# Kernel optimization log

Measured on AMD Instinct MI355X. Metric: run time of the kernel, lower is better.

The kernel has to match this reference:

```python
import jax, jax.numpy as jnp
import numpy as np

B, P, K = 128, 1024, 4  # 128 clouds of 1024 points, kNN k=4 (includes self, as PyG knn does)


def _edge_mlp(e, W1, b1, W2, b2):
    # PyG MLP([2d, c, c]) with plain_last=True: ReLU after first linear only;
    # batch-norm at init (running_mean=0, var=1) is identity in eval mode.
    h = jax.nn.relu(e @ W1 + b1)
    return h @ W2 + b2


def _dynamic_edge_conv(x, W1, b1, W2, b2):
    # x: [B, P, d]. Recompute kNN graph in feature space per cloud, build edge
    # features [x_i, x_j - x_i], apply MLP, max-aggregate over neighbors.
    sq = jnp.sum(x * x, axis=-1)  # [B,P]
    dist = sq[:, :, None] + sq[:, None, :] - 2.0 * jnp.einsum('bid,bjd->bij', x, x)  # [B,P,P]
    _, idx = jax.lax.top_k(-dist, K)  # [B,P,K] nearest neighbors (self included, dist 0)
    xj = jax.vmap(lambda xc, ic: xc[ic])(x, idx)  # [B,P,K,d]
    xi = jnp.broadcast_to(x[:, :, None, :], xj.shape)
    e = jnp.concatenate([xi, xj - xi], axis=-1)  # [B,P,K,2d]
    h = _edge_mlp(e, W1, b1, W2, b2)  # [B,P,K,c]
    return jnp.max(h, axis=2)  # max aggregation -> [B,P,c]


def setup_inputs() -> dict:
    key = jax.random.key(0)
    ks = jax.random.split(key, 24)
    s = 0.1
    d = {
        'x': jax.random.normal(ks[0], (B * P, 1), dtype=jnp.float32),
        'batch': (jnp.arange(B * P, dtype=jnp.int32) // P),
        # conv1: MLP([2, 32, 32])
        'c1W1': s * jax.random.normal(ks[1], (2, 32)), 'c1b1': jnp.zeros((32,)),
        'c1W2': s * jax.random.normal(ks[2], (32, 32)), 'c1b2': jnp.zeros((32,)),
        # conv2: MLP([64, 32, 32])
        'c2W1': s * jax.random.normal(ks[3], (64, 32)), 'c2b1': jnp.zeros((32,)),
        'c2W2': s * jax.random.normal(ks[4], (32, 32)), 'c2b2': jnp.zeros((32,)),
        # conv3: MLP([64, 64, 64])
        'c3W1': s * jax.random.normal(ks[5], (64, 64)), 'c3b1': jnp.zeros((64,)),
        'c3W2': s * jax.random.normal(ks[6], (64, 64)), 'c3b2': jnp.zeros((64,)),
        # final MLP([128, 264, 264, 264, 2]), norm=None, dropout inactive in eval
        'mW1': s * jax.random.normal(ks[7], (128, 264)), 'mb1': jnp.zeros((264,)),
        'mW2': s * jax.random.normal(ks[8], (264, 264)), 'mb2': jnp.zeros((264,)),
        'mW3': s * jax.random.normal(ks[9], (264, 264)), 'mb3': jnp.zeros((264,)),
        'mW4': s * jax.random.normal(ks[10], (264, 2)), 'mb4': jnp.zeros((2,)),
    }
    return d


def reference(x, batch, c1W1, c1b1, c1W2, c1b2, c2W1, c2b1, c2W2, c2b2,
              c3W1, c3b1, c3W2, c3b2, mW1, mb1, mW2, mb2, mW3, mb3, mW4, mb4):
    # batch ids are contiguous equal-size groups (arange // P); use reshape.
    xb = x.reshape(B, P, -1)
    x1 = _dynamic_edge_conv(xb, c1W1, c1b1, c1W2, c1b2)  # [B,P,32]
    x2 = _dynamic_edge_conv(x1, c2W1, c2b1, c2W2, c2b2)  # [B,P,32]
    x3 = _dynamic_edge_conv(x2, c3W1, c3b1, c3W2, c3b2)  # [B,P,64]
    f = jnp.concatenate([x1, x2, x3], axis=-1).reshape(B * P, -1)  # [N,128]
    h = jax.nn.relu(f @ mW1 + mb1)
    h = jax.nn.relu(h @ mW2 + mb2)
    h = jax.nn.relu(h @ mW3 + mb3)
    out = h @ mW4 + mb4  # [N,2]
    return jax.nn.log_softmax(out, axis=1)
```

## Files before the change

### kernel.cpp

```cpp
#include <hip/hip_runtime.h>
#include <hip/hip_bf16.h>
#include <float.h>
#include <math.h>

#define BB 128
#define PP 1024
#define KNN 4
#define NROWS (BB * PP)

typedef __bf16 v8bf __attribute__((ext_vector_type(8)));
typedef float  v4f  __attribute__((ext_vector_type(4)));

__device__ inline unsigned short f2bs(float f) {
    __hip_bfloat16 h = __float2bfloat16(f);
    return *(unsigned short*)&h;
}
__device__ inline unsigned packbf2(float a, float b) {
    return (unsigned)f2bs(a) | ((unsigned)f2bs(b) << 16);
}
__device__ inline float bflo(unsigned u) { return __builtin_bit_cast(float, u << 16); }
__device__ inline float bfhi(unsigned u) { return __builtin_bit_cast(float, u & 0xFFFF0000u); }

__global__ __launch_bounds__(256)
void pack_kernel(const float* __restrict__ src, int D,
                 __hip_bfloat16* __restrict__ xh, __hip_bfloat16* __restrict__ xl,
                 float* __restrict__ sq)
{
    const int t = blockIdx.x * 256 + threadIdx.x;
    const int row = t >> 2, part = t & 3;
    float v[8];
    #pragma unroll
    for (int u = 0; u < 8; u++) {
        int d = part * 8 + u;
        v[u] = (d < D) ? src[(size_t)row * D + d] : 0.f;
    }
    float s = 0.f;
    unsigned int hw[4], lw[4];
    #pragma unroll
    for (int w = 0; w < 4; w++) {
        unsigned short h2[2], l2[2];
        #pragma unroll
        for (int e = 0; e < 2; e++) {
            float x = v[2 * w + e];
            __hip_bfloat16 hb = __float2bfloat16(x);
            float hf = __bfloat162float(hb);
            __hip_bfloat16 lb = __float2bfloat16(x - hf);
            h2[e] = *(unsigned short*)&hb;
            l2[e] = *(unsigned short*)&lb;
            s = fmaf(x, x, s);
        }
        hw[w] = (unsigned int)h2[0] | ((unsigned int)h2[1] << 16);
        lw[w] = (unsigned int)l2[0] | ((unsigned int)l2[1] << 16);
    }
    s += __shfl_xor(s, 1);
    s += __shfl_xor(s, 2);
    uint4 hv; hv.x = hw[0]; hv.y = hw[1]; hv.z = hw[2]; hv.w = hw[3];
    uint4 lv; lv.x = lw[0]; lv.y = lw[1]; lv.z = lw[2]; lv.w = lw[3];
    *(uint4*)&xh[(size_t)row * 32 + part * 8] = hv;
    *(uint4*)&xl[(size_t)row * 32 + part * 8] = lv;
    if (part == 0) sq[row] = s;
}

__global__ __launch_bounds__(256, 4)
void knn_mfma(const __hip_bfloat16* __restrict__ xh, const __hip_bfloat16* __restrict__ xl,
              const float* __restrict__ sq, int* __restrict__ nidx)
{
    __shared__ __align__(16) char scb[64 * 512];
    unsigned* cand = (unsigned*)scb;

    const int tid = threadIdx.x;
    const int wv = tid >> 6, lane = tid & 63;
    const int lr = lane & 15, lq = lane >> 4;
    const int b = blockIdx.y, i0 = blockIdx.x * 64;
    const size_t Rb = (size_t)b * PP;

    v8bf ah[4], al[4];
    #pragma unroll
    for (int it = 0; it < 4; it++) {
        size_t g = Rb + i0 + it * 16 + lr;
        ah[it] = __builtin_bit_cast(v8bf, *(const uint4*)(xh + g * 32 + lq * 8));
        al[it] = __builtin_bit_cast(v8bf, *(const uint4*)(xl + g * 32 + lq * 8));
    }

    float sqq[4][4];
    #pragma unroll
    for (int it = 0; it < 4; it++)
        #pragma unroll
        for (int m = 0; m < 4; m++)
            sqq[it][m] = sq[Rb + i0 + it * 16 + lq * 4 + m];

    const int r = tid & 63, qt = tid >> 6;
    unsigned m0 = ~0u, m1 = ~0u, m2 = ~0u, m3 = ~0u;

    for (int ch = 0; ch < 8; ch++) {
        #pragma unroll
        for (int jt2 = 0; jt2 < 2; jt2++) {
            const int tl = wv * 2 + jt2;
            const size_t gj = Rb + ch * 128 + tl * 16 + lr;
            v8bf bh = __builtin_bit_cast(v8bf, *(const uint4*)(xh + gj * 32 + lq * 8));
            v8bf bl = __builtin_bit_cast(v8bf, *(const uint4*)(xl + gj * 32 + lq * 8));
            const float sqv = sq[gj];
            const unsigned jloc = (unsigned)(ch * 128 + tl * 16 + lr);
            const int cb = (tl * 16 + lr) * 4;
            #pragma unroll
            for (int it = 0; it < 4; it++) {
                v4f a = (v4f){0.f, 0.f, 0.f, 0.f};
                a = __builtin_amdgcn_mfma_f32_16x16x32_bf16(al[it], bl, a, 0, 0, 0);
                a = __builtin_amdgcn_mfma_f32_16x16x32_bf16(al[it], bh, a, 0, 0, 0);
                a = __builtin_amdgcn_mfma_f32_16x16x32_bf16(ah[it], bl, a, 0, 0, 0);
                a = __builtin_amdgcn_mfma_f32_16x16x32_bf16(ah[it], bh, a, 0, 0, 0);
                #pragma unroll
                for (int m = 0; m < 4; m++) {
                    float s = fmaf(-2.f, a[m], sqv + sqq[it][m]);
                    s = fmaxf(s, 0.f);
                    unsigned key = (__builtin_bit_cast(unsigned, s) & 0xFFFFFC00u) | jloc;
                    const int row = it * 16 + lq * 4 + m;
                    *(unsigned*)(scb + row * 512 + (cb ^ ((row & 7) << 4))) = key;
                }
            }
        }
        __asm__ volatile("" ::: "memory");
        {
            const int rsw = (r & 7) << 4;
            #pragma unroll
            for (int s8 = 0; s8 < 8; s8++) {
                uint4 kv = *(const uint4*)(scb + r * 512 + ((qt * 128 + s8 * 16) ^ rsw));
                unsigned kk[4] = {kv.x, kv.y, kv.z, kv.w};
                #pragma unroll
                for (int e = 0; e < 4; e++) {
                    unsigned key = kk[e], t;
                    t = min(m0, key); key = max(m0, key); m0 = t;
                    t = min(m1, key); key = max(m1, key); m1 = t;
                    t = min(m2, key); key = max(m2, key); m2 = t;
                    m3 = min(m3, key);
                }
            }
        }
        __asm__ volatile("" ::: "memory");
    }

    __syncthreads();
    cand[(qt * 4 + 0) * 64 + r] = m0;
    cand[(qt * 4 + 1) * 64 + r] = m1;
    cand[(qt * 4 + 2) * 64 + r] = m2;
    cand[(qt * 4 + 3) * 64 + r] = m3;
    __syncthreads();

    if (tid < 64) {
        unsigned g0 = ~0u, g1 = ~0u, g2 = ~0u, g3 = ~0u;
        #pragma unroll
        for (int s2 = 0; s2 < 16; s2++) {
            unsigned key = cand[s2 * 64 + tid], t;
            t = min(g0, key); key = max(g0, key); g0 = t;
            t = min(g1, key); key = max(g1, key); g1 = t;
            t = min(g2, key); key = max(g2, key); g2 = t;
            g3 = min(g3, key);
        }
        const int base = (int)Rb;
        int* op = nidx + (size_t)(Rb + i0 + tid) * KNN;
        op[0] = base + (int)(g0 & 1023u);
        op[1] = base + (int)(g1 & 1023u);
        op[2] = base + (int)(g2 & 1023u);
        op[3] = base + (int)(g3 & 1023u);
    }
}

template<int D, int H, int C, typename OT>
__global__ __launch_bounds__(256, 4)
void edge_mfma(const float* __restrict__ x, const int* __restrict__ nidx,
               const __hip_bfloat16* __restrict__ EW1, const __hip_bfloat16* __restrict__ EW2,
               const float* __restrict__ b1g, const float* __restrict__ b2g,
               OT* __restrict__ out)
{
    constexpr int NE = 256;
    constexpr int TDP = (D == 1) ? 32 : 64;
    constexpr int DP  = TDP / 2;
    constexpr int P   = ((TDP > H) ? TDP : H) + 8;
    constexpr int NT1 = H / 16, NT2 = C / 16;
    constexpr int KS1 = TDP / 32, KS2 = H / 32;

    __shared__ __hip_bfloat16 xe[NE * P];

    const int tid = threadIdx.x;
    const int wv = tid >> 6, lane = tid & 63;
    const int lr = lane & 15, q = lane >> 4;
    const int p0 = blockIdx.x * 64;

    {
        const int e = wv * 64 + lane;
        const int j = nidx[(size_t)p0 * KNN + e];
        const int pi = p0 + (e >> 2);
        if constexpr (D == 1) {
            #pragma unroll
            for (int s = 0; s < P / 8; s++) {
                uint4 z; z.x = 0u; z.y = 0u; z.z = 0u; z.w = 0u;
                *(uint4*)&xe[e * P + s * 8] = z;
            }
            xe[e * P + 0]  = __float2bfloat16(x[pi]);
            xe[e * P + DP] = __float2bfloat16(x[j]);
        } else {
            const float* si = x + (size_t)pi * D;
            const float* sj = x + (size_t)j * D;
            #pragma unroll
            for (int s = 0; s < D / 8; s++) {
                float4 f0 = *(const float4*)&si[s * 8];
                float4 f1 = *(const float4*)&si[s * 8 + 4];
                uint4 uv;
                uv.x = packbf2(f0.x, f0.y); uv.y = packbf2(f0.z, f0.w);
                uv.z = packbf2(f1.x, f1.y); uv.w = packbf2(f1.z, f1.w);
                *(uint4*)&xe[e * P + s * 8] = uv;
            }
            #pragma unroll
            for (int s = 0; s < D / 8; s++) {
                float4 f0 = *(const float4*)&sj[s * 8];
                float4 f1 = *(const float4*)&sj[s * 8 + 4];
                uint4 uv;
                uv.x = packbf2(f0.x, f0.y); uv.y = packbf2(f0.z, f0.w);
                uv.z = packbf2(f1.x, f1.y); uv.w = packbf2(f1.z, f1.w);
                *(uint4*)&xe[e * P + DP + s * 8] = uv;
            }
        }
    }

    v4f acc1[4][NT1];
    #pragma unroll
    for (int mi = 0; mi < 4; mi++)
        #pragma unroll
        for (int nt = 0; nt < NT1; nt++) acc1[mi][nt] = (v4f){0.f, 0.f, 0.f, 0.f};

    #pragma unroll
    for (int ks = 0; ks < KS1; ks++) {
        v8bf a[4];
        #pragma unroll
        for (int mi = 0; mi < 4; mi++)
            a[mi] = __builtin_bit_cast(v8bf,
                *(const uint4*)&xe[(wv * 64 + mi * 16 + lr) * P + ks * 32 + q * 8]);
        v8bf b[NT1];
        #pragma unroll
        for (int nt = 0; nt < NT1; nt++)
            b[nt] = __builtin_bit_cast(v8bf,
                *(const uint4*)(EW1 + (size_t)(nt * 16 + lr) * TDP + ks * 32 + q * 8));
        #pragma unroll
        for (int mi = 0; mi < 4; mi++)
            #pragma unroll
            for (int nt = 0; nt < NT1; nt++)
                acc1[mi][nt] = __builtin_amdgcn_mfma_f32_16x16x32_bf16(a[mi], b[nt], acc1[mi][nt], 0, 0, 0);
    }
    #pragma unroll
    for (int nt = 0; nt < NT1; nt++) {
        const float bias = b1g[nt * 16 + lr];
        #pragma unroll
        for (int mi = 0; mi < 4; mi++) {
            #pragma unroll
            for (int m = 0; m < 4; m++) {
                int row = wv * 64 + mi * 16 + q * 4 + m;
                xe[row * P + nt * 16 + lr] =
                    __float2bfloat16(fmaxf(acc1[mi][nt][m] + bias, 0.f));
            }
        }
    }

    v4f acc2[4][NT2];
    #pragma unroll
    for (int mi = 0; mi < 4; mi++)
        #pragma unroll
        for (int nt = 0; nt < NT2; nt++) acc2[mi][nt] = (v4f){0.f, 0.f, 0.f, 0.f};

    #pragma unroll
    for (int ks = 0; ks < KS2; ks++) {
        v8bf a[4];
        #pragma unroll
        for (int mi = 0; mi < 4; mi++)
            a[mi] = __builtin_bit_cast(v8bf,
                *(const uint4*)&xe[(wv * 64 + mi * 16 + lr) * P + ks * 32 + q * 8]);
        v8bf b[NT2];
        #pragma unroll
        for (int nt = 0; nt < NT2; nt++)
            b[nt] = __builtin_bit_cast(v8bf,
                *(const uint4*)(EW2 + (size_t)(nt * 16 + lr) * H + ks * 32 + q * 8));
        #pragma unroll
        for (int mi = 0; mi < 4; mi++)
            #pragma unroll
            for (int nt = 0; nt < NT2; nt++)
                acc2[mi][nt] = __builtin_amdgcn_mfma_f32_16x16x32_bf16(a[mi], b[nt], acc2[mi][nt], 0, 0, 0);
    }
    #pragma unroll
    for (int nt = 0; nt < NT2; nt++) {
        const int c = nt * 16 + lr;
        const float bias = b2g[c];
        #pragma unroll
        for (int mi = 0; mi < 4; mi++) {
            float v = fmaxf(fmaxf(acc2[mi][nt][0], acc2[mi][nt][1]),
                            fmaxf(acc2[mi][nt][2], acc2[mi][nt][3])) + bias;
            const int p = p0 + (wv * 4 + mi) * 4 + q;
            if constexpr (sizeof(OT) == 4) out[(size_t)p * C + c] = v;
            else                           out[(size_t)p * C + c] = __float2bfloat16(v);
        }
    }
}

__global__ void prep_kernel(const float* __restrict__ mW1, const float* __restrict__ mW2,
                            const float* __restrict__ mW3,
                            const float* __restrict__ mb1, const float* __restrict__ mb2,
                            const float* __restrict__ mb3,
                            const float* __restrict__ c1W1, const float* __restrict__ c1W2,
                            const float* __restrict__ c2W1, const float* __restrict__ c2W2,
                            const float* __restrict__ c3W1, const float* __restrict__ c3W2,
                            __hip_bfloat16* __restrict__ WT1, __hip_bfloat16* __restrict__ WT2,
                            __hip_bfloat16* __restrict__ WT3, float* __restrict__ bp,
                            __hip_bfloat16* __restrict__ E11, __hip_bfloat16* __restrict__ E12,
                            __hip_bfloat16* __restrict__ E13,
                            __hip_bfloat16* __restrict__ E21, __hip_bfloat16* __restrict__ E22,
                            __hip_bfloat16* __restrict__ E23)
{
    const int t0 = blockIdx.x * blockDim.x + threadIdx.x;
    const int NT = gridDim.x * blockDim.x;
    for (int i = t0; i < 272 * 136; i += NT) {
        int n = i / 136, k = i - n * 136;
        WT1[i] = (n < 264 && k < 128) ? __float2bfloat16(mW1[(size_t)k * 264 + n]) : __float2bfloat16(0.f);
    }
    for (int i = t0; i < 272 * 296; i += NT) {
        int n = i / 296, k = i - n * 296;
        WT2[i] = (n < 264 && k < 264) ? __float2bfloat16(mW2[(size_t)k * 264 + n]) : __float2bfloat16(0.f);
        WT3[i] = (n < 264 && k < 264) ? __float2bfloat16(mW3[(size_t)k * 264 + n]) : __float2bfloat16(0.f);
    }
    for (int i = t0; i < 3 * 272; i += NT) {
        int l = i / 272, n = i - l * 272;
        const float* bsrc = (l == 0) ? mb1 : (l == 1) ? mb2 : mb3;
        bp[i] = (n < 264) ? bsrc[n] : 0.f;
    }
    for (int i = t0; i < 32 * 32; i += NT) {
        int h = i >> 5, k = i & 31;
        float v = (k == 0) ? (c1W1[h] - c1W1[32 + h]) : (k == 16 ? c1W1[32 + h] : 0.f);
        E11[i] = __float2bfloat16(v);
    }
    for (int i = t0; i < 32 * 64; i += NT) {
        int h = i >> 6, k = i & 63;
        float v = (k < 32) ? (c2W1[k * 32 + h] - c2W1[(k + 32) * 32 + h]) : c2W1[k * 32 + h];
        E12[i] = __float2bfloat16(v);
    }
    for (int i = t0; i < 64 * 64; i += NT) {
        int h = i >> 6, k = i & 63;
        float v = (k < 32) ? (c3W1[k * 64 + h] - c3W1[(k + 32) * 64 + h]) : c3W1[k * 64 + h];
        E13[i] = __float2bfloat16(v);
    }
    for (int i = t0; i < 32 * 32; i += NT) {
        int c = i >> 5, h = i & 31;
        E21[i] = __float2bfloat16(c1W2[h * 32 + c]);
        E22[i] = __float2bfloat16(c2W2[h * 32 + c]);
    }
    for (int i = t0; i < 64 * 64; i += NT) {
        int c = i >> 6, h = i & 63;
        E23[i] = __float2bfloat16(c3W2[h * 64 + c]);
    }
}

#define ACT_RB 640

template<int NK>
__device__ __forceinline__ void mlp_layer(
    char* actb, const __hip_bfloat16* __restrict__ WT, const int KP,
    const float* __restrict__ bias, const int wv, const int rlane, const int ph)
{
    v4f acc[4][4], acc16;
    #pragma unroll
    for (int i = 0; i < 4; i++)
        #pragma unroll
        for (int rt = 0; rt < 4; rt++) acc[i][rt] = (v4f){0.f, 0.f, 0.f, 0.f};
    acc16 = (v4f){0.f, 0.f, 0.f, 0.f};

    const int sw = (rlane & 7) << 4;
    const __hip_bfloat16* wbase = WT + (size_t)rlane * KP + ph * 8;

    v8bf wb[2][5];
    auto loadW = [&](int ks, int buf) {
        #pragma unroll
        for (int i = 0; i < 4; i++)
            wb[buf][i] = __builtin_bit_cast(v8bf,
                *(const uint4*)(wbase + (size_t)(wv + 4 * i) * 16 * KP + ks * 32));
        wb[buf][4] = __builtin_bit_cast(v8bf,
                *(const uint4*)(wbase + (size_t)256 * KP + ks * 32));
    };
    loadW(0, 0);

    #pragma unroll
    for (int ks = 0; ks < NK; ks++) {
        const int cur = ks & 1;
        if (ks + 1 < NK) loadW(ks + 1, cur ^ 1);
        v8bf ab[4], ab16;
        #pragma unroll
        for (int rt = 0; rt < 4; rt++)
            ab[rt] = __builtin_bit_cast(v8bf,
                *(const uint4*)(actb + (rt * 16 + rlane) * ACT_RB + ((ks * 64 + ph * 16) ^ sw)));
        ab16 = __builtin_bit_cast(v8bf,
                *(const uint4*)(actb + (wv * 16 + rlane) * ACT_RB + ((ks * 64 + ph * 16) ^ sw)));
        #pragma unroll
        for (int i = 0; i < 4; i++)
            #pragma unroll
            for (int rt = 0; rt < 4; rt++)
                acc[i][rt] = __builtin_amdgcn_mfma_f32_16x16x32_bf16(wb[cur][i], ab[rt], acc[i][rt], 0, 0, 0);
        acc16 = __builtin_amdgcn_mfma_f32_16x16x32_bf16(wb[cur][4], ab16, acc16, 0, 0, 0);
    }
    __syncthreads();

    #pragma unroll
    for (int i = 0; i < 4; i++) {
        const int col0 = (wv + 4 * i) * 16 + ph * 4;
        const float4 bv = *(const float4*)&bias[col0];
        #pragma unroll
        for (int rt = 0; rt < 4; rt++) {
            const int row = rt * 16 + rlane;
            ushort4 pk;
            pk.x = f2bs(fmaxf(acc[i][rt][0] + bv.x, 0.f));
            pk.y = f2bs(fmaxf(acc[i][rt][1] + bv.y, 0.f));
            pk.z = f2bs(fmaxf(acc[i][rt][2] + bv.z, 0.f));
            pk.w = f2bs(fmaxf(acc[i][rt][3] + bv.w, 0.f));
            *(ushort4*)(actb + row * ACT_RB + ((col0 * 2) ^ ((rlane & 7) << 4))) = pk;
        }
    }
    {
        const int col0 = 256 + ph * 4;
        const float4 bv = *(const float4*)&bias[col0];
        const int row = wv * 16 + rlane;
        ushort4 pk;
        pk.x = f2bs(fmaxf(acc16[0] + bv.x, 0.f));
        pk.y = f2bs(fmaxf(acc16[1] + bv.y, 0.f));
        pk.z = f2bs(fmaxf(acc16[2] + bv.z, 0.f));
        pk.w = f2bs(fmaxf(acc16[3] + bv.w, 0.f));
        *(ushort4*)(actb + row * ACT_RB + ((col0 * 2) ^ ((rlane & 7) << 4))) = pk;
    }
    __syncthreads();
}

__global__ __launch_bounds__(256, 3)
void mlp_kernel(const float* __restrict__ x1, const float* __restrict__ x2,
                const __hip_bfloat16* __restrict__ x3,
                const __hip_bfloat16* __restrict__ WT1, const __hip_bfloat16* __restrict__ WT2,
                const __hip_bfloat16* __restrict__ WT3, const float* __restrict__ bp,
                const float* __restrict__ mW4, const float* __restrict__ mb4,
                float* __restrict__ outp)
{
    __shared__ __align__(16) char actb[64 * ACT_RB];
    __shared__ __align__(16) float W4s[264 * 2 + 2];
    __shared__ float lsm[64 * 2];

    const int tid = threadIdx.x;
    const int wv = tid >> 6, lane = tid & 63;
    const int rlane = lane & 15, ph = lane >> 4;
    const size_t row0 = (size_t)blockIdx.x * 64;

    {
        uint4 z; z.x = 0u; z.y = 0u; z.z = 0u; z.w = 0u;
        for (int t = tid; t < 64 * 6; t += 256) {
            int r = t / 6, s = t - r * 6;
            int cb = (34 + s) * 16;
            *(uint4*)(actb + r * ACT_RB + (cb ^ ((r & 7) << 4))) = z;
        }
        for (int t = tid; t < 64 * 8; t += 256) {
            int r = t >> 3, g = t & 7;
            size_t grow = row0 + r;
            const int swr = (r & 7) << 4;
            float4 fa = *(const float4*)&x1[grow * 32 + g * 4];
            uint2 ua; ua.x = packbf2(fa.x, fa.y); ua.y = packbf2(fa.z, fa.w);
            *(uint2*)(actb + r * ACT_RB + ((g * 8) ^ swr)) = ua;
            float4 fb = *(const float4*)&x2[grow * 32 + g * 4];
            uint2 ub; ub.x = packbf2(fb.x, fb.y); ub.y = packbf2(fb.z, fb.w);
            *(uint2*)(actb + r * ACT_RB + ((64 + g * 8) ^ swr)) = ub;
            uint4 uc = *(const uint4*)&x3[grow * 64 + g * 8];
            *(uint4*)(actb + r * ACT_RB + ((128 + g * 16) ^ swr)) = uc;
        }
        for (int t = tid; t < 530; t += 256) {
            if (t < 528) { int c = t / 264, k2 = t - c * 264; W4s[t] = mW4[(size_t)k2 * 2 + c]; }
            else W4s[t] = mb4[t - 528];
        }
    }
    __syncthreads();

    mlp_layer<4>(actb, WT1, 136, bp,       wv, rlane, ph);
    mlp_layer<9>(actb, WT2, 296, bp + 272, wv, rlane, ph);
    mlp_layer<9>(actb, WT3, 296, bp + 544, wv, rlane, ph);

    if (tid < 128) {
        int r = tid >> 1, c = tid & 1;
        const float* wp = &W4s[c * 264];
        const int swr = (r & 7) << 4;
        float s = 0.f;
        for (int k = 0; k < 264; k += 8) {
            uint4 u = *(const uint4*)(actb + r * ACT_RB + ((2 * k) ^ swr));
            float4 wa = *(const float4*)&wp[k];
            float4 wb2 = *(const float4*)&wp[k + 4];
            s = fmaf(bflo(u.x), wa.x, s); s = fmaf(bfhi(u.x), wa.y, s);
            s = fmaf(bflo(u.y), wa.z, s); s = fmaf(bfhi(u.y), wa.w, s);
            s = fmaf(bflo(u.z), wb2.x, s); s = fmaf(bfhi(u.z), wb2.y, s);
            s = fmaf(bflo(u.w), wb2.z, s); s = fmaf(bfhi(u.w), wb2.w, s);
        }
        lsm[tid] = s + W4s[528 + c];
    }
    __syncthreads();
    if (tid < 64) {
        float l0 = lsm[tid * 2 + 0], l1 = lsm[tid * 2 + 1];
        float m = fmaxf(l0, l1);
        float lse = m + logf(expf(l0 - m) + expf(l1 - m));
        float2 o; o.x = l0 - lse; o.y = l1 - lse;
        *(float2*)&outp[(row0 + tid) * 2] = o;
    }
}

extern "C" void kernel_launch(void* const* d_in, const int* in_sizes, int n_in,
                              void* d_out, int out_size, void* d_ws, size_t ws_size,
                              hipStream_t stream)
{
    const float* x    = (const float*)d_in[0];
    const float* c1W1 = (const float*)d_in[2];
    const float* c1b1 = (const float*)d_in[3];
    const float* c1W2 = (const float*)d_in[4];
    const float* c1b2 = (const float*)d_in[5];
    const float* c2W1 = (const float*)d_in[6];
    const float* c2b1 = (const float*)d_in[7];
    const float* c2W2 = (const float*)d_in[8];
    const float* c2b2 = (const float*)d_in[9];
    const float* c3W1 = (const float*)d_in[10];
    const float* c3b1 = (const float*)d_in[11];
    const float* c3W2 = (const float*)d_in[12];
    const float* c3b2 = (const float*)d_in[13];
    const float* mW1  = (const float*)d_in[14];
    const float* mb1  = (const float*)d_in[15];
    const float* mW2  = (const float*)d_in[16];
    const float* mb2  = (const float*)d_in[17];
    const float* mW3  = (const float*)d_in[18];
    const float* mb3  = (const float*)d_in[19];
    const float* mW4  = (const float*)d_in[20];
    const float* mb4  = (const float*)d_in[21];

    float* x1 = (float*)d_ws;
    float* x2 = x1 + (size_t)NROWS * 32;
    __hip_bfloat16* x3 = (__hip_bfloat16*)(x2 + (size_t)NROWS * 32);
    int* nidx = (int*)(x3 + (size_t)NROWS * 64);
    __hip_bfloat16* WT1 = (__hip_bfloat16*)(nidx + (size_t)NROWS * 4);
    __hip_bfloat16* WT2 = WT1 + 272 * 136;
    __hip_bfloat16* WT3 = WT2 + 272 * 296;
    float* bp = (float*)(WT3 + 272 * 296);
    __hip_bfloat16* xph = (__hip_bfloat16*)(bp + 3 * 272);
    __hip_bfloat16* xpl = xph + (size_t)NROWS * 32;
    float* sqw = (float*)(xpl + (size_t)NROWS * 32);
    __hip_bfloat16* E11 = (__hip_bfloat16*)(sqw + NROWS);
    __hip_bfloat16* E12 = E11 + 32 * 32;
    __hip_bfloat16* E13 = E12 + 32 * 64;
    __hip_bfloat16* E21 = E13 + 64 * 64;
    __hip_bfloat16* E22 = E21 + 32 * 32;
    __hip_bfloat16* E23 = E22 + 32 * 32;

    prep_kernel<<<dim3(512), 256, 0, stream>>>(mW1, mW2, mW3, mb1, mb2, mb3,
                                               c1W1, c1W2, c2W1, c2W2, c3W1, c3W2,
                                               WT1, WT2, WT3, bp,
                                               E11, E12, E13, E21, E22, E23);

    dim3 kgrid(PP / 64, BB);
    dim3 pgrid(NROWS * 4 / 256);
    dim3 egrid(NROWS / 64);

    pack_kernel<<<pgrid, 256, 0, stream>>>(x, 1, xph, xpl, sqw);
    knn_mfma<<<kgrid, 256, 0, stream>>>(xph, xpl, sqw, nidx);
    edge_mfma<1, 32, 32, float><<<egrid, 256, 0, stream>>>(x, nidx, E11, E21, c1b1, c1b2, x1);

    pack_kernel<<<pgrid, 256, 0, stream>>>(x1, 32, xph, xpl, sqw);
    knn_mfma<<<kgrid, 256, 0, stream>>>(xph, xpl, sqw, nidx);
    edge_mfma<32, 32, 32, float><<<egrid, 256, 0, stream>>>(x1, nidx, E12, E22, c2b1, c2b2, x2);

    pack_kernel<<<pgrid, 256, 0, stream>>>(x2, 32, xph, xpl, sqw);
    knn_mfma<<<kgrid, 256, 0, stream>>>(xph, xpl, sqw, nidx);
    edge_mfma<32, 64, 64, __hip_bfloat16><<<egrid, 256, 0, stream>>>(x2, nidx, E13, E23, c3b1, c3b2, x3);

    mlp_kernel<<<dim3(NROWS / 64), 256, 0, stream>>>(x1, x2, x3, WT1, WT2, WT3, bp,
                                                     mW4, mb4, (float*)d_out);
}
```

Measured before the change: 440.1 us.

## Split MLP kernel work across eight waves instead of four

Doubles the MLP kernel block to 512 threads (8 waves), so each wave computes 2 column tiles instead of 4, and the extra 16-column tail tile is handled only by waves 4-7. The final 264->2 projection is split into four partial sums per output, reduced through shared memory, and fast exp/log intrinsics replace the precise ones. The aim is more waves per CU to hide latency and less register pressure per wave, at the cost of a larger block, different launch bounds, and some imbalance between waves.

Result: no change. 437.3 us (-0.6%).

```diff
diff --git a/kernel.cpp b/kernel.cpp
--- a/kernel.cpp
+++ b/kernel.cpp
@@ -362,23 +362,26 @@
     char* actb, const __hip_bfloat16* __restrict__ WT, const int KP,
     const float* __restrict__ bias, const int wv, const int rlane, const int ph)
 {
-    v4f acc[4][4], acc16;
-    #pragma unroll
-    for (int i = 0; i < 4; i++)
+    v4f acc[2][4], acc16;
+    #pragma unroll
+    for (int i = 0; i < 2; i++)
         #pragma unroll
         for (int rt = 0; rt < 4; rt++) acc[i][rt] = (v4f){0.f, 0.f, 0.f, 0.f};
     acc16 = (v4f){0.f, 0.f, 0.f, 0.f};
 
     const int sw = (rlane & 7) << 4;
     const __hip_bfloat16* wbase = WT + (size_t)rlane * KP + ph * 8;
-
-    v8bf wb[2][5];
+    const bool has16 = (wv >= 4);
+    const int r16 = ((wv - 4) & 3) * 16 + rlane;
+
+    v8bf wb[2][2], wb16[2];
     auto loadW = [&](int ks, int buf) {
-        #pragma unroll
-        for (int i = 0; i < 4; i++)
-            wb[buf][i] = __builtin_bit_cast(v8bf,
-                *(const uint4*)(wbase + (size_t)(wv + 4 * i) * 16 * KP + ks * 32));
-        wb[buf][4] = __builtin_bit_cast(v8bf,
+        wb[buf][0] = __builtin_bit_cast(v8bf,
+            *(const uint4*)(wbase + (size_t)wv * 16 * KP + ks * 32));
+        wb[buf][1] = __builtin_bit_cast(v8bf,
+            *(const uint4*)(wbase + (size_t)(8 + wv) * 16 * KP + ks * 32));
+        if (has16)
+            wb16[buf] = __builtin_bit_cast(v8bf,
                 *(const uint4*)(wbase + (size_t)256 * KP + ks * 32));
     };
     loadW(0, 0);
@@ -392,20 +395,22 @@
         for (int rt = 0; rt < 4; rt++)
             ab[rt] = __builtin_bit_cast(v8bf,
                 *(const uint4*)(actb + (rt * 16 + rlane) * ACT_RB + ((ks * 64 + ph * 16) ^ sw)));
-        ab16 = __builtin_bit_cast(v8bf,
-                *(const uint4*)(actb + (wv * 16 + rlane) * ACT_RB + ((ks * 64 + ph * 16) ^ sw)));
-        #pragma unroll
-        for (int i = 0; i < 4; i++)
+        if (has16)
+            ab16 = __builtin_bit_cast(v8bf,
+                *(const uint4*)(actb + r16 * ACT_RB + ((ks * 64 + ph * 16) ^ sw)));
+        #pragma unroll
+        for (int i = 0; i < 2; i++)
             #pragma unroll
             for (int rt = 0; rt < 4; rt++)
                 acc[i][rt] = __builtin_amdgcn_mfma_f32_16x16x32_bf16(wb[cur][i], ab[rt], acc[i][rt], 0, 0, 0);
-        acc16 = __builtin_amdgcn_mfma_f32_16x16x32_bf16(wb[cur][4], ab16, acc16, 0, 0, 0);
+        if (has16)
+            acc16 = __builtin_amdgcn_mfma_f32_16x16x32_bf16(wb16[cur], ab16, acc16, 0, 0, 0);
     }
     __syncthreads();
 
     #pragma unroll
-    for (int i = 0; i < 4; i++) {
-        const int col0 = (wv + 4 * i) * 16 + ph * 4;
+    for (int i = 0; i < 2; i++) {
+        const int col0 = (wv + 8 * i) * 16 + ph * 4;
         const float4 bv = *(const float4*)&bias[col0];
         #pragma unroll
         for (int rt = 0; rt < 4; rt++) {
@@ -418,21 +423,20 @@
             *(ushort4*)(actb + row * ACT_RB + ((col0 * 2) ^ ((rlane & 7) << 4))) = pk;
         }
     }
-    {
+    if (has16) {
         const int col0 = 256 + ph * 4;
         const float4 bv = *(const float4*)&bias[col0];
-        const int row = wv * 16 + rlane;
         ushort4 pk;
         pk.x = f2bs(fmaxf(acc16[0] + bv.x, 0.f));
         pk.y = f2bs(fmaxf(acc16[1] + bv.y, 0.f));
         pk.z = f2bs(fmaxf(acc16[2] + bv.z, 0.f));
         pk.w = f2bs(fmaxf(acc16[3] + bv.w, 0.f));
-        *(ushort4*)(actb + row * ACT_RB + ((col0 * 2) ^ ((rlane & 7) << 4))) = pk;
+        *(ushort4*)(actb + r16 * ACT_RB + ((col0 * 2) ^ ((rlane & 7) << 4))) = pk;
     }
     __syncthreads();
 }
 
-__global__ __launch_bounds__(256, 3)
+__global__ __launch_bounds__(512, 4)
 void mlp_kernel(const float* __restrict__ x1, const float* __restrict__ x2,
                 const __hip_bfloat16* __restrict__ x3,
                 const __hip_bfloat16* __restrict__ WT1, const __hip_bfloat16* __restrict__ WT2,
@@ -442,7 +446,7 @@
 {
     __shared__ __align__(16) char actb[64 * ACT_RB];
     __shared__ __align__(16) float W4s[264 * 2 + 2];
-    __shared__ float lsm[64 * 2];
+    __shared__ float lsm[512];
 
     const int tid = threadIdx.x;
     const int wv = tid >> 6, lane = tid & 63;
@@ -451,12 +455,12 @@
 
     {
         uint4 z; z.x = 0u; z.y = 0u; z.z = 0u; z.w = 0u;
-        for (int t = tid; t < 64 * 6; t += 256) {
+        for (int t = tid; t < 64 * 6; t += 512) {
             int r = t / 6, s = t - r * 6;
             int cb = (34 + s) * 16;
             *(uint4*)(actb + r * ACT_RB + (cb ^ ((r & 7) << 4))) = z;
         }
-        for (int t = tid; t < 64 * 8; t += 256) {
+        for (int t = tid; t < 64 * 8; t += 512) {
             int r = t >> 3, g = t & 7;
             size_t grow = row0 + r;
             const int swr = (r & 7) << 4;
@@ -469,7 +473,7 @@
             uint4 uc = *(const uint4*)&x3[grow * 64 + g * 8];
             *(uint4*)(actb + r * ACT_RB + ((128 + g * 16) ^ swr)) = uc;
         }
-        for (int t = tid; t < 530; t += 256) {
+        for (int t = tid; t < 530; t += 512) {
             if (t < 528) { int c = t / 264, k2 = t - c * 264; W4s[t] = mW4[(size_t)k2 * 2 + c]; }
             else W4s[t] = mb4[t - 528];
         }
@@ -480,12 +484,15 @@
     mlp_layer<9>(actb, WT2, 296, bp + 272, wv, rlane, ph);
     mlp_layer<9>(actb, WT3, 296, bp + 544, wv, rlane, ph);
 
-    if (tid < 128) {
-        int r = tid >> 1, c = tid & 1;
+    {
+        const int r = tid >> 3, rem = tid & 7;
+        const int c = rem >> 2, h = rem & 3;
         const float* wp = &W4s[c * 264];
         const int swr = (r & 7) << 4;
+        const int k0 = (h == 0) ? 0 : (8 + 64 * h);
+        const int k1 = k0 + ((h == 0) ? 72 : 64);
         float s = 0.f;
-        for (int k = 0; k < 264; k += 8) {
+        for (int k = k0; k < k1; k += 8) {
             uint4 u = *(const uint4*)(actb + r * ACT_RB + ((2 * k) ^ swr));
             float4 wa = *(const float4*)&wp[k];
             float4 wb2 = *(const float4*)&wp[k + 4];
@@ -494,13 +501,14 @@
             s = fmaf(bflo(u.z), wb2.x, s); s = fmaf(bfhi(u.z), wb2.y, s);
             s = fmaf(bflo(u.w), wb2.z, s); s = fmaf(bfhi(u.w), wb2.w, s);
         }
-        lsm[tid] = s + W4s[528 + c];
+        lsm[tid] = s;
     }
     __syncthreads();
     if (tid < 64) {
-        float l0 = lsm[tid * 2 + 0], l1 = lsm[tid * 2 + 1];
+        float l0 = lsm[tid * 8 + 0] + lsm[tid * 8 + 1] + lsm[tid * 8 + 2] + lsm[tid * 8 + 3] + W4s[528];
+        float l1 = lsm[tid * 8 + 4] + lsm[tid * 8 + 5] + lsm[tid * 8 + 6] + lsm[tid * 8 + 7] + W4s[529];
         float m = fmaxf(l0, l1);
-        float lse = m + logf(expf(l0 - m) + expf(l1 - m));
+        float lse = m + __logf(__expf(l0 - m) + __expf(l1 - m));
         float2 o; o.x = l0 - lse; o.y = l1 - lse;
         *(float2*)&outp[(row0 + tid) * 2] = o;
     }
@@ -571,6 +579,6 @@
     knn_mfma<<<kgrid, 256, 0, stream>>>(xph, xpl, sqw, nidx);
     edge_mfma<32, 64, 64, __hip_bfloat16><<<egrid, 256, 0, stream>>>(x2, nidx, E13, E23, c3b1, c3b2, x3);
 
-    mlp_kernel<<<dim3(NROWS / 64), 256, 0, stream>>>(x1, x2, x3, WT1, WT2, WT3, bp,
+    mlp_kernel<<<dim3(NROWS / 64), 512, 0, stream>>>(x1, x2, x3, WT1, WT2, WT3, bp,
                                                      mW4, mb4, (float*)d_out);
 }
```
